# Performance work log

Measured on AMD Instinct MI355X. Metric: run time of the kernel, lower is better.

## Reference

```python
import jax, jax.numpy as jnp
import numpy as np

B = 1; T = 2048; H = 2048; NH = 16; KVH = 4; HD = 128; WIN = 512; SINK = 64
S = 64; NG = 4; MLP_I = 5504; CK = 4
INTER = NH * HD; CONV_DIM = INTER + 2 * NG * S; NPROJ = INTER + CONV_DIM + NH
EPS = 1e-6; MEPS = 1e-5


def rmsnorm(x, w, eps):
    return x * jax.lax.rsqrt(jnp.mean(x * x, -1, keepdims=True) + eps) * w


def rotate_half(x):
    h = x.shape[-1] // 2
    return jnp.concatenate([-x[..., h:], x[..., :h]], -1)


def setup_inputs():
    key = jax.random.key(0)
    ks = jax.random.split(key, 32)
    rn = lambda k, s, sc=0.02: jax.random.normal(k, s, dtype=jnp.float32) * sc
    inv = 1.0 / (10000.0 ** (np.arange(0, HD, 2, dtype=np.float64) / HD))
    fr = np.outer(np.arange(T), inv)
    emb = np.concatenate([fr, fr], -1)
    return {
        'hidden_states': jax.random.normal(ks[0], (B, T, H), dtype=jnp.float32),
        'cos': jnp.asarray(np.cos(emb), jnp.float32)[None],
        'sin': jnp.asarray(np.sin(emb), jnp.float32)[None],
        'ln1_w': jnp.ones((H,), jnp.float32),
        'q_w': rn(ks[1], (NH * HD, H)), 'q_b': rn(ks[2], (NH * HD,)),
        'k_w': rn(ks[3], (KVH * HD, H)), 'k_b': rn(ks[4], (KVH * HD,)),
        'v_w': rn(ks[5], (KVH * HD, H)), 'v_b': rn(ks[6], (KVH * HD,)),
        'o_w': rn(ks[7], (H, NH * HD)),
        'in_proj_w': rn(ks[8], (NPROJ, H)),
        'conv_w': rn(ks[9], (CONV_DIM, 1, CK), 0.1),
        'conv_b': rn(ks[10], (CONV_DIM,), 0.1),
        'dt_bias': rn(ks[11], (NH,), 0.5),
        'A_log': rn(ks[12], (NH,), 0.5),
        'D': rn(ks[13], (NH,), 0.5),
        'mnorm_w': jnp.ones((INTER,), jnp.float32),
        'out_proj_w': rn(ks[14], (H, INTER)),
        'ln2_w': jnp.ones((H,), jnp.float32),
        'gate_w': rn(ks[15], (MLP_I, H)),
        'up_w': rn(ks[16], (MLP_I, H)),
        'down_w': rn(ks[17], (H, MLP_I)),
    }


def _mamba2(ev, in_proj_w, conv_w, conv_b, dt_bias, A_log, D, mnorm_w, out_proj_w):
    # ev: [B, L, H] evicted hidden states; Mamba2 with expand=1 (intermediate=INTER)
    L = ev.shape[1]
    proj = jnp.einsum('blh,ph->blp', ev, in_proj_w)
    z = proj[..., :INTER]
    xBC = proj[..., INTER:INTER + CONV_DIM]
    dt = proj[..., INTER + CONV_DIM:]
    # depthwise causal conv1d, kernel 4
    xBC = jax.lax.conv_general_dilated(
        xBC.transpose(0, 2, 1), conv_w, (1,), [(CK - 1, 0)],
        dimension_numbers=('NCH', 'OIH', 'NCH'), feature_group_count=CONV_DIM)
    xBC = jax.nn.silu((xBC + conv_b[None, :, None]).transpose(0, 2, 1))
    x = xBC[..., :INTER].reshape(B, L, NH, HD)
    Bm = jnp.repeat(xBC[..., INTER:INTER + NG * S].reshape(B, L, NG, S), NH // NG, axis=2)
    Cm = jnp.repeat(xBC[..., INTER + NG * S:].reshape(B, L, NG, S), NH // NG, axis=2)
    dt = jax.nn.softplus(dt + dt_bias)  # [B, L, NH]
    A = -jnp.exp(A_log)  # [NH]

    def scan_one(xb, bb, cb, db):
        def step(state, inp):
            xt, bt, ct, dtt = inp  # [NH,HD],[NH,S],[NH,S],[NH]
            decay = jnp.exp(dtt * A)[:, None, None]
            state = decay * state + (dtt[:, None] * xt)[..., None] * bt[:, None, :]
            y = jnp.einsum('hds,hs->hd', state, ct) + D[:, None] * xt
            return state, y
        _, ys = jax.lax.scan(step, jnp.zeros((NH, HD, S), xb.dtype), (xb, bb, cb, db))
        return ys

    y = jax.vmap(scan_one)(x, Bm, Cm, dt).reshape(B, L, INTER)
    g = y * jax.nn.silu(z)  # gated RMSNorm
    g = g * jax.lax.rsqrt(jnp.mean(g * g, -1, keepdims=True) + MEPS) * mnorm_w
    return jnp.einsum('bli,hi->blh', g, out_proj_w)


def reference(hidden_states, cos, sin, ln1_w, q_w, q_b, k_w, k_b, v_w, v_b, o_w,
              in_proj_w, conv_w, conv_b, dt_bias, A_log, D, mnorm_w, out_proj_w,
              ln2_w, gate_w, up_w, down_w):
    pre = rmsnorm(hidden_states, ln1_w, EPS)  # input_layernorm
    evict_end = T - WIN
    mem_out = _mamba2(pre[:, SINK:evict_end, :], in_proj_w, conv_w, conv_b,
                      dt_bias, A_log, D, mnorm_w, out_proj_w)  # [B, Le, H]
    mem_act = mem_out[:, -1:, :]

    def qkv(x, w, b, nh):
        return (jnp.einsum('blh,ph->blp', x, w) + b).reshape(x.shape[0], x.shape[1], nh, HD).transpose(0, 2, 1, 3)

    q = qkv(pre, q_w, q_b, NH)
    k = qkv(pre, k_w, k_b, KVH)
    v = qkv(pre, v_w, v_b, KVH)
    c = cos[:, None]; s = sin[:, None]
    q = q * c + rotate_half(q) * s
    k = k * c + rotate_half(k) * s
    # mem token injection at position SINK (mem projections are not rotated)
    q = q.at[:, :, SINK, :].set(qkv(mem_act, q_w, q_b, NH)[:, :, 0, :])
    k = k.at[:, :, SINK, :].set(qkv(mem_act, k_w, k_b, KVH)[:, :, 0, :])
    v = v.at[:, :, SINK, :].set(qkv(mem_act, v_w, v_b, KVH)[:, :, 0, :])
    # sink + sliding-window causal mask with mem-token bias
    row = jnp.arange(T)[:, None]; col = jnp.arange(T)[None, :]
    protected = SINK + 1
    bad = (col > row) | ((col < row - WIN) & (col >= protected))
    minv = jnp.finfo(jnp.float32).min
    mask = jnp.where(bad, minv, 0.0)[None, None]
    le_fact = (T - SINK - WIN) / T
    mask = mask.at[..., SINK].add(0.5 * le_fact)
    rep = NH // KVH
    kf = jnp.repeat(k, rep, axis=1)
    vf = jnp.repeat(v, rep, axis=1)
    scores = jnp.einsum('bhqd,bhkd->bhqk', q, kf) * (HD ** -0.5) + mask
    attn = jax.nn.softmax(scores, axis=-1)
    o = jnp.einsum('bhqk,bhkd->bhqd', attn, vf).transpose(0, 2, 1, 3).reshape(B, T, NH * HD)
    # training-path merge: sinks | mem_out | window
    merged = jnp.concatenate([o[:, :SINK], mem_out, o[:, T - WIN:]], axis=1)
    attn_out = jnp.einsum('blp,hp->blh', merged, o_w)
    h = hidden_states + attn_out
    m = rmsnorm(h, ln2_w, EPS)
    mlp = jnp.einsum('bli,hi->blh',
                     jax.nn.silu(jnp.einsum('blh,ih->bli', m, gate_w)) * jnp.einsum('blh,ih->bli', m, up_w),
                     down_w)
    return h + mlp
```

## Files before the change

### kernel.cpp

```cpp
#include <hip/hip_runtime.h>
#include <hip/hip_bf16.h>

#define TSEQ   2048
#define HDIM   2048
#define NHEAD  16
#define KVHEAD 4
#define HEADD  128
#define WINSZ  512
#define SINKN  64
#define MLPI   5504
#define CONVD  2560
#define NPROJD 4624
#define LMEM   1472
#define NCHUNK 23
#define QKVD   3072

typedef unsigned short bf_t;
typedef __attribute__((ext_vector_type(8))) short short8;
typedef __attribute__((ext_vector_type(4))) short s4v;
typedef __attribute__((ext_vector_type(4))) float ffrag;

#define BOF_PRE   0ull
#define BOF_QKV   8388608ull
#define BOF_P     8388608ull
#define BOF_S     20447232ull
#define BOF_PROJ  33554432ull
#define BOF_GB    33554432ull
#define BOF_XBCC  60780544ull
#define BOF_GF    75853824ull
#define BOF_MERG  75853824ull
#define BOF_GN    87912448ull
#define BOF_H     93941760ull
#define BOF_DT    110718976ull
#define BOF_GA    110813184ull
#define BOF_FLAG  110907392ull
#define BOF_LC    110908416ull

#define BOF_CNV_A 8388608ull
#define BOF_CNV_B 60780544ull

__device__ __forceinline__ float bf2f(bf_t x) { return __uint_as_float(((unsigned)x) << 16); }
__device__ __forceinline__ bf_t f2bf(float x) {
  unsigned u = __float_as_uint(x);
  return (bf_t)((u + 0x7FFFu + ((u >> 16) & 1u)) >> 16);
}
__device__ __forceinline__ float ldin(const void* p, size_t i, int bf) {
  if (bf) return bf2f(((const bf_t*)p)[i]);
  return ((const float*)p)[i];
}
__device__ __forceinline__ float siluf(float x) { return x / (1.f + expf(-x)); }

typedef const __attribute__((address_space(1))) unsigned gl_u32;
typedef __attribute__((address_space(3))) unsigned lds_u32;
__device__ __forceinline__ void gld16(const void* g, void* l) {
  __builtin_amdgcn_global_load_lds((gl_u32*)g, (lds_u32*)l, 16, 0, 0);
}

__device__ __forceinline__ void xcd_swz(int gx, int gy, int& x, int& y) {
  int id = blockIdx.y * gx + blockIdx.x;
  int total = gx * gy;
  int xcd = id & 7, j = id >> 3;
  int q = total >> 3, r = total & 7;
  int w = (xcd < r ? xcd*(q+1) : r*(q+1) + (xcd-r)*q) + j;
  x = w / gy;
  y = w % gy;
}

__global__ void detect_k(const void* __restrict__ ln1, int* __restrict__ flag) {
  unsigned w0 = *(const unsigned*)ln1;
  *flag = (w0 == 0x3F803F80u) ? 1 : 0;
}

__global__ __launch_bounds__(256) void wconv_k(const float* __restrict__ src,
    bf_t* __restrict__ dst, int n8, const int* __restrict__ flagp) {
  if (*flagp) return;
  int idx = blockIdx.x*256 + threadIdx.x;
  if (idx >= n8) return;
  const float* s = src + (size_t)idx*8;
  float4 a = *(const float4*)s, b = *(const float4*)(s+4);
  short8 o;
  o[0]=(short)f2bf(a.x); o[1]=(short)f2bf(a.y); o[2]=(short)f2bf(a.z); o[3]=(short)f2bf(a.w);
  o[4]=(short)f2bf(b.x); o[5]=(short)f2bf(b.y); o[6]=(short)f2bf(b.z); o[7]=(short)f2bf(b.w);
  *(short8*)(dst + (size_t)idx*8) = o;
}

__global__ __launch_bounds__(256) void rms_in_k(const void* __restrict__ x,
    const void* __restrict__ w, bf_t* __restrict__ out, float eps,
    const int* __restrict__ flagp) {
  int bf = *flagp;
  int row = blockIdx.x, tid = threadIdx.x;
  float v[8];
  if (bf) {
    const bf_t* xr = (const bf_t*)x + (size_t)row*HDIM + tid*8;
#pragma unroll
    for (int j = 0; j < 8; ++j) v[j] = bf2f(xr[j]);
  } else {
    const float* xr = (const float*)x + (size_t)row*HDIM + tid*8;
    float4 a = *(const float4*)xr, b = *(const float4*)(xr+4);
    v[0]=a.x; v[1]=a.y; v[2]=a.z; v[3]=a.w; v[4]=b.x; v[5]=b.y; v[6]=b.z; v[7]=b.w;
  }
  float ss = 0.f;
#pragma unroll
  for (int j = 0; j < 8; ++j) ss += v[j]*v[j];
  __shared__ float red[256];
  red[tid] = ss; __syncthreads();
  for (int s = 128; s > 0; s >>= 1) { if (tid < s) red[tid] += red[tid+s]; __syncthreads(); }
  float scale = 1.f / sqrtf(red[0]*(1.f/HDIM) + eps);
  bf_t* o = out + (size_t)row*HDIM + tid*8;
#pragma unroll
  for (int j = 0; j < 8; ++j) o[j] = f2bf(v[j]*scale*ldin(w, tid*8+j, bf));
}

__global__ __launch_bounds__(256) void rms_f2b_k(const float* __restrict__ x,
    const void* __restrict__ w, bf_t* __restrict__ out, float eps,
    const int* __restrict__ flagp) {
  int bf = *flagp;
  int row = blockIdx.x, tid = threadIdx.x;
  const float* xr = x + (size_t)row*2048 + tid*8;
  float4 a = *(const float4*)xr, b = *(const float4*)(xr+4);
  float v[8] = {a.x,a.y,a.z,a.w,b.x,b.y,b.z,b.w};
  float ss = 0.f;
#pragma unroll
  for (int j = 0; j < 8; ++j) ss += v[j]*v[j];
  __shared__ float red[256];
  red[tid] = ss; __syncthreads();
  for (int s = 128; s > 0; s >>= 1) { if (tid < s) red[tid] += red[tid+s]; __syncthreads(); }
  float scale = 1.f / sqrtf(red[0]*(1.f/2048.f) + eps);
  bf_t* o = out + (size_t)row*2048 + tid*8;
#pragma unroll
  for (int j = 0; j < 8; ++j) o[j] = f2bf(v[j]*scale*ldin(w, tid*8+j, bf));
}

__global__ __launch_bounds__(256) void tgemm_k(
    const bf_t* __restrict__ A, int lda,
    const void* __restrict__ W0, const void* __restrict__ W1, const void* __restrict__ W2,
    const bf_t* __restrict__ C0, const bf_t* __restrict__ C1, const bf_t* __restrict__ C2,
    int ldw, int n1, int n2,
    const void* __restrict__ b0, const void* __restrict__ b1, const void* __restrict__ b2,
    const void* __restrict__ res,
    const float* __restrict__ hf,
    void* __restrict__ out,
    int ldc, int M, int N, int K, int mode, int outbf,
    const int* __restrict__ flagp) {
  int bf = *flagp;
  __shared__ short As[8192];
  __shared__ short Bs[4096];
  int tid = threadIdx.x;
  int lane = tid & 63, wv = tid >> 6;
  int sx, sy; xcd_swz(gridDim.x, gridDim.y, sx, sy);
  int bm = sy << 7, bn = sx << 6;

  int trow = tid >> 2;
  int kc = (((tid & 3) ^ ((tid >> 3) & 3)) << 3);
  int ar0 = bm + trow;        if (ar0 > M-1) ar0 = M-1;
  int ar1 = bm + 64 + trow;   if (ar1 > M-1) ar1 = M-1;
  int wr  = bn + trow;        if (wr > N-1) wr = N-1;
  const bf_t* ga0 = A + (size_t)ar0*lda + kc;
  const bf_t* ga1 = A + (size_t)ar1*lda + kc;
  const bf_t* w0 = bf ? (const bf_t*)W0 : C0;
  const bf_t* w1 = bf ? (const bf_t*)W1 : C1;
  const bf_t* w2 = bf ? (const bf_t*)W2 : C2;
  const bf_t* Wsel; int wrl;
  if (wr < n1)      { Wsel = w0; wrl = wr; }
  else if (wr < n2) { Wsel = w1; wrl = wr - n1; }
  else              { Wsel = w2; wrl = wr - n2; }
  const bf_t* gwb = Wsel + (size_t)wrl*ldw + kc;
  int sA = wv*512;

  int wm = (wv & 1) << 6, wn = (wv >> 1) << 5;
  int fr = lane & 15;
  int fq = (((lane >> 4) ^ ((fr >> 1) & 3)) << 3);

  ffrag acc[4][2];
#pragma unroll
  for (int i = 0; i < 4; ++i)
#pragma unroll
    for (int j = 0; j < 2; ++j) acc[i][j] = (ffrag){0.f,0.f,0.f,0.f};

  int nst = K >> 5;
  gld16(ga0, As + sA);
  gld16(ga1, As + 2048 + sA);
  gld16(gwb, Bs + sA);
  gld16(ga0 + 32, As + 4096 + sA);
  gld16(ga1 + 32, As + 4096 + 2048 + sA);
  gld16(gwb + 32, Bs + 2048 + sA);

  for (int t = 0; t < nst; ++t) {
    if (t + 1 < nst) { asm volatile("s_waitcnt vmcnt(3)" ::: "memory"); }
    else             { asm volatile("s_waitcnt vmcnt(0)" ::: "memory"); }
    __builtin_amdgcn_s_barrier();
    int cbA = (t & 1) << 12, cbB = (t & 1) << 11;
    short8 af[4], bfr[2];
#pragma unroll
    for (int i = 0; i < 4; ++i)
      af[i] = *(const short8*)&As[cbA + (wm + i*16 + fr)*32 + fq];
#pragma unroll
    for (int j = 0; j < 2; ++j)
      bfr[j] = *(const short8*)&Bs[cbB + (wn + j*16 + fr)*32 + fq];
    asm volatile("s_waitcnt lgkmcnt(0)" ::: "memory");
    __builtin_amdgcn_s_barrier();
    int nxt = (t + 2) << 5;
    if (nxt < K) {
      gld16(ga0 + nxt, As + cbA + sA);
      gld16(ga1 + nxt, As + cbA + 2048 + sA);
      gld16(gwb + nxt, Bs + cbB + sA);
    }
#pragma unroll
    for (int i = 0; i < 4; ++i)
#pragma unroll
      for (int j = 0; j < 2; ++j)
        acc[i][j] = __builtin_amdgcn_mfma_f32_16x16x32_bf16(af[i], bfr[j], acc[i][j], 0, 0, 0);
  }

  int rbase = (lane >> 4) << 2;
  int cbase = lane & 15;
#pragma unroll
  for (int i = 0; i < 4; ++i) {
#pragma unroll
    for (int j = 0; j < 2; ++j) {
#pragma unroll
      for (int r = 0; r < 4; ++r) {
        int m = bm + wm + i*16 + rbase + r;
        int n = bn + wn + j*16 + cbase;
        if (m >= M || n >= N) continue;
        size_t ci = (size_t)m*ldc + n;
        float v = acc[i][j][r];
        if (mode == 0) {
          if (b0) {
            if (n < n1)      v += ldin(b0, n, bf);
            else if (n < n2) v += ldin(b1, n - n1, bf);
            else             v += ldin(b2, n - n2, bf);
          }
          if (outbf) ((bf_t*)out)[ci] = f2bf(v); else ((float*)out)[ci] = v;
        } else if (mode == 1) {
          ((float*)out)[ci] = v + ldin(res, ci, bf);
        } else {
          float hv = hf[ci] + v;
          if (bf) ((bf_t*)out)[ci] = f2bf(hv); else ((float*)out)[ci] = hv;
        }
      }
    }
  }
}

__global__ __launch_bounds__(256, 2) void fgemm_k(
    const bf_t* __restrict__ A, int lda,
    const void* __restrict__ Wg, const void* __restrict__ Wu,
    const bf_t* __restrict__ Cg, const bf_t* __restrict__ Cu, int ldw,
    bf_t* __restrict__ out, int M, int N, int K,
    const int* __restrict__ flagp) {
  int bf = *flagp;
  __shared__ short As[8192];
  __shared__ short Bg[8192];
  __shared__ short Bu[8192];
  int tid = threadIdx.x;
  int lane = tid & 63, wv = tid >> 6;
  int sx, sy; xcd_swz(gridDim.x, gridDim.y, sx, sy);
  int bm = sy << 7, bn = sx << 7;

  int trow = tid >> 2;
  int kc = (((tid & 3) ^ ((tid >> 3) & 3)) << 3);
  int ar0 = bm + trow;        if (ar0 > M-1) ar0 = M-1;
  int ar1 = bm + 64 + trow;   if (ar1 > M-1) ar1 = M-1;
  const bf_t* ga0 = A + (size_t)ar0*lda + kc;
  const bf_t* ga1 = A + (size_t)ar1*lda + kc;
  const bf_t* wg = bf ? (const bf_t*)Wg : Cg;
  const bf_t* wu = bf ? (const bf_t*)Wu : Cu;
  const bf_t* gg0 = wg + (size_t)(bn + trow)*ldw + kc;
  const bf_t* gg1 = wg + (size_t)(bn + 64 + trow)*ldw + kc;
  const bf_t* gu0 = wu + (size_t)(bn + trow)*ldw + kc;
  const bf_t* gu1 = wu + (size_t)(bn + 64 + trow)*ldw + kc;
  int sA = wv*512;

  int wm = (wv & 1) << 6, wn = (wv >> 1) << 6;
  int fr = lane & 15;
  int fq = (((lane >> 4) ^ ((fr >> 1) & 3)) << 3);

  ffrag ag[4][4], au[4][4];
#pragma unroll
  for (int i = 0; i < 4; ++i)
#pragma unroll
    for (int j = 0; j < 4; ++j) { ag[i][j] = (ffrag){0.f,0.f,0.f,0.f}; au[i][j] = (ffrag){0.f,0.f,0.f,0.f}; }

  int nst = K >> 5;
  gld16(ga0, As + sA);
  gld16(ga1, As + 2048 + sA);
  gld16(gg0, Bg + sA);
  gld16(gg1, Bg + 2048 + sA);
  gld16(gu0, Bu + sA);
  gld16(gu1, Bu + 2048 + sA);
  gld16(ga0 + 32, As + 4096 + sA);
  gld16(ga1 + 32, As + 4096 + 2048 + sA);
  gld16(gg0 + 32, Bg + 4096 + sA);
  gld16(gg1 + 32, Bg + 4096 + 2048 + sA);
  gld16(gu0 + 32, Bu + 4096 + sA);
  gld16(gu1 + 32, Bu + 4096 + 2048 + sA);

  for (int t = 0; t < nst; ++t) {
    if (t + 1 < nst) { asm volatile("s_waitcnt vmcnt(6)" ::: "memory"); }
    else             { asm volatile("s_waitcnt vmcnt(0)" ::: "memory"); }
    __builtin_amdgcn_s_barrier();
    int cb = (t & 1) << 12;
    short8 af[4], bgf[4], buf2[4];
#pragma unroll
    for (int i = 0; i < 4; ++i)
      af[i] = *(const short8*)&As[cb + (wm + i*16 + fr)*32 + fq];
#pragma unroll
    for (int j = 0; j < 4; ++j) {
      bgf[j]  = *(const short8*)&Bg[cb + (wn + j*16 + fr)*32 + fq];
      buf2[j] = *(const short8*)&Bu[cb + (wn + j*16 + fr)*32 + fq];
    }
    asm volatile("s_waitcnt lgkmcnt(0)" ::: "memory");
    __builtin_amdgcn_s_barrier();
    int nxt = (t + 2) << 5;
    if (nxt < K) {
      gld16(ga0 + nxt, As + cb + sA);
      gld16(ga1 + nxt, As + cb + 2048 + sA);
      gld16(gg0 + nxt, Bg + cb + sA);
      gld16(gg1 + nxt, Bg + cb + 2048 + sA);
      gld16(gu0 + nxt, Bu + cb + sA);
      gld16(gu1 + nxt, Bu + cb + 2048 + sA);
    }
#pragma unroll
    for (int i = 0; i < 4; ++i)
#pragma unroll
      for (int j = 0; j < 4; ++j) {
        ag[i][j] = __builtin_amdgcn_mfma_f32_16x16x32_bf16(af[i], bgf[j],  ag[i][j], 0, 0, 0);
        au[i][j] = __builtin_amdgcn_mfma_f32_16x16x32_bf16(af[i], buf2[j], au[i][j], 0, 0, 0);
      }
  }

  int rbase = (lane >> 4) << 2;
  int cbase = lane & 15;
#pragma unroll
  for (int i = 0; i < 4; ++i)
#pragma unroll
    for (int j = 0; j < 4; ++j)
#pragma unroll
      for (int r = 0; r < 4; ++r) {
        int m = bm + wm + i*16 + rbase + r;
        int n = bn + wn + j*16 + cbase;
        if (m >= M || n >= N) continue;
        float g = ag[i][j][r], u = au[i][j][r];
        out[(size_t)m*N + n] = f2bf(siluf(g) * u);
      }
}

__global__ __launch_bounds__(256) void rope_k(float* __restrict__ tb, int stride,
    const void* __restrict__ cosp, const void* __restrict__ sinp,
    int nheads, const int* __restrict__ flagp) {
  int bf = *flagp;
  int idx = blockIdx.x*256 + threadIdx.x;
  int d = idx & 63;
  int rem = idx >> 6;
  int tpos = rem / nheads, hh = rem % nheads;
  float* base = tb + (size_t)tpos*stride + hh*128;
  float a = base[d], b = base[d+64];
  float c0 = ldin(cosp, (size_t)tpos*128 + d, bf),    s0 = ldin(sinp, (size_t)tpos*128 + d, bf);
  float c1 = ldin(cosp, (size_t)tpos*128 + d + 64, bf), s1 = ldin(sinp, (size_t)tpos*128 + d + 64, bf);
  base[d]    = a*c0 - b*s0;
  base[d+64] = b*c1 + a*s1;
}

__global__ __launch_bounds__(256) void conv_k(const float* __restrict__ proj,
    const void* __restrict__ convw, const void* __restrict__ convb,
    float* __restrict__ xbcc, const int* __restrict__ flagp) {
  int bf = *flagp;
  int idx = blockIdx.x*256 + threadIdx.x;
  int t = idx / CONVD, c = idx % CONVD;
  float acc = ldin(convb, c, bf);
#pragma unroll
  for (int j = 0; j < 4; ++j) {
    int tt = t - 3 + j;
    if (tt >= 0) acc += ldin(convw, (size_t)c*4 + j, bf) * proj[(size_t)tt*NPROJD + 2048 + c];
  }
  xbcc[idx] = siluf(acc);
}

__global__ __launch_bounds__(256) void dt_k(const float* __restrict__ proj,
    const void* __restrict__ dtb, const void* __restrict__ alog,
    float* __restrict__ dtv, float* __restrict__ ga, const int* __restrict__ flagp) {
  int bf = *flagp;
  int idx = blockIdx.x*256 + threadIdx.x;
  int t = idx >> 4, h = idx & 15;
  float raw = proj[(size_t)t*NPROJD + 4608 + h] + ldin(dtb, h, bf);
  float dt = (raw > 30.f) ? raw : log1pf(expf(raw));
  float A = -expf(ldin(alog, h, bf));
  dtv[idx] = dt;
  ga[idx] = dt*A;
}

__global__ __launch_bounds__(256) void cums_k(const float* __restrict__ ga,
    float* __restrict__ Lc) {
  int wid = blockIdx.x*4 + (threadIdx.x >> 6);
  int lane = threadIdx.x & 63;
  int h = wid / NCHUNK, c = wid % NCHUNK;
  int t = c*64 + lane;
  float a = ga[(size_t)t*16 + h];
#pragma unroll
  for (int off = 1; off < 64; off <<= 1) {
    float o = __shfl_up(a, off, 64);
    if (lane >= off) a += o;
  }
  Lc[(size_t)(h*NCHUNK + c)*64 + lane] = a;
}

__global__ __launch_bounds__(256) void chunkstate_k(
    const float* __restrict__ xbcc, const float* __restrict__ dtv,
    const float* __restrict__ Lc, float* __restrict__ Pbuf) {
  __shared__ short XT[128*72];
  __shared__ short BT[64*72];
  __shared__ float wj[64];
  int tid = threadIdx.x, lane = tid & 63, wv = tid >> 6;
  int b = blockIdx.x;
  int h = b & 15, c = b >> 4;
  int g64 = (h >> 2) << 6;
  size_t hc = (size_t)(h*NCHUNK + c);

  if (tid < 64) {
    float L63 = Lc[hc*64 + 63];
    float Lj  = Lc[hc*64 + tid];
    wj[tid] = dtv[(size_t)(c*64 + tid)*16 + h] * expf(L63 - Lj);
  }
  __syncthreads();
  for (int base = tid*4; base < 8192; base += 1024) {
    int j = base >> 7, d = base & 127;
    float4 xv = *(const float4*)&xbcc[(size_t)(c*64 + j)*CONVD + h*128 + d];
    XT[(d+0)*72 + j] = (short)f2bf(xv.x);
    XT[(d+1)*72 + j] = (short)f2bf(xv.y);
    XT[(d+2)*72 + j] = (short)f2bf(xv.z);
    XT[(d+3)*72 + j] = (short)f2bf(xv.w);
  }
  for (int base = tid*4; base < 4096; base += 1024) {
    int j = base >> 6, s = base & 63;
    float w = wj[j];
    float4 bv = *(const float4*)&xbcc[(size_t)(c*64 + j)*CONVD + 2048 + g64 + s];
    BT[(s+0)*72 + j] = (short)f2bf(bv.x * w);
    BT[(s+1)*72 + j] = (short)f2bf(bv.y * w);
    BT[(s+2)*72 + j] = (short)f2bf(bv.z * w);
    BT[(s+3)*72 + j] = (short)f2bf(bv.w * w);
  }
  __syncthreads();

  int fr = lane & 15, fq = (lane >> 4) << 3;
  ffrag acc[2][4];
#pragma unroll
  for (int i = 0; i < 2; ++i)
#pragma unroll
    for (int j = 0; j < 4; ++j) acc[i][j] = (ffrag){0.f,0.f,0.f,0.f};
#pragma unroll
  for (int k0 = 0; k0 < 64; k0 += 32) {
    short8 af[2], bfr[4];
#pragma unroll
    for (int i = 0; i < 2; ++i)
      af[i] = *(const short8*)&XT[(wv*32 + i*16 + fr)*72 + k0 + fq];
#pragma unroll
    for (int j = 0; j < 4; ++j)
      bfr[j] = *(const short8*)&BT[(j*16 + fr)*72 + k0 + fq];
#pragma unroll
    for (int i = 0; i < 2; ++i)
#pragma unroll
      for (int j = 0; j < 4; ++j)
        acc[i][j] = __builtin_amdgcn_mfma_f32_16x16x32_bf16(af[i], bfr[j], acc[i][j], 0, 0, 0);
  }
  int rbase = (lane >> 4) << 2, cbase = lane & 15;
#pragma unroll
  for (int i = 0; i < 2; ++i)
#pragma unroll
    for (int j = 0; j < 4; ++j)
#pragma unroll
      for (int r = 0; r < 4; ++r) {
        int d = wv*32 + i*16 + rbase + r;
        int s = j*16 + cbase;
        Pbuf[hc*8192 + d*64 + s] = acc[i][j][r];
      }
}

__global__ __launch_bounds__(256) void statepass_k(
    const float* __restrict__ Pbuf, const float* __restrict__ Lc,
    float* __restrict__ Sbuf) {
  int gid = blockIdx.x*256 + threadIdx.x;
  int h = gid >> 13, rem = gid & 8191;
  float s = 0.f;
  for (int c = 0; c < NCHUNK; ++c) {
    size_t hc = (size_t)(h*NCHUNK + c);
    Sbuf[hc*8192 + rem] = s;
    s = expf(Lc[hc*64 + 63]) * s + Pbuf[hc*8192 + rem];
  }
}

__global__ __launch_bounds__(256) void chunkout_k(
    const float* __restrict__ xbcc, const float* __restrict__ proj,
    const float* __restrict__ dtv, const float* __restrict__ Lc,
    const float* __restrict__ Sbuf, const void* __restrict__ Dp,
    float* __restrict__ g, const int* __restrict__ flagp) {
  __shared__ short Cs[64*72];
  __shared__ short BsS[64*72];
  __shared__ short XT[128*72];
  __shared__ short Sinb[128*72];
  __shared__ float Lch[64];
  __shared__ float dtch[64];
  int bf = *flagp;
  int tid = threadIdx.x, lane = tid & 63, wv = tid >> 6;
  int b = blockIdx.x;
  int h = b & 15, c = b >> 4;
  int g64 = (h >> 2) << 6;
  size_t hc = (size_t)(h*NCHUNK + c);
  float Dh = ldin(Dp, h, bf);

  if (tid < 64) {
    Lch[tid]  = Lc[hc*64 + tid];
    dtch[tid] = dtv[(size_t)(c*64 + tid)*16 + h];
  }
  for (int base = tid*4; base < 4096; base += 1024) {
    int i = base >> 6, s = base & 63;
    float4 cv = *(const float4*)&xbcc[(size_t)(c*64 + i)*CONVD + 2304 + g64 + s];
    Cs[i*72 + s+0] = (short)f2bf(cv.x); Cs[i*72 + s+1] = (short)f2bf(cv.y);
    Cs[i*72 + s+2] = (short)f2bf(cv.z); Cs[i*72 + s+3] = (short)f2bf(cv.w);
    float4 bv = *(const float4*)&xbcc[(size_t)(c*64 + i)*CONVD + 2048 + g64 + s];
    BsS[i*72 + s+0] = (short)f2bf(bv.x); BsS[i*72 + s+1] = (short)f2bf(bv.y);
    BsS[i*72 + s+2] = (short)f2bf(bv.z); BsS[i*72 + s+3] = (short)f2bf(bv.w);
  }
  for (int base = tid*4; base < 8192; base += 1024) {
    int j = base >> 7, d = base & 127;
    float4 xv = *(const float4*)&xbcc[(size_t)(c*64 + j)*CONVD + h*128 + d];
    XT[(d+0)*72 + j] = (short)f2bf(xv.x);
    XT[(d+1)*72 + j] = (short)f2bf(xv.y);
    XT[(d+2)*72 + j] = (short)f2bf(xv.z);
    XT[(d+3)*72 + j] = (short)f2bf(xv.w);
  }
  for (int base = tid*4; base < 8192; base += 1024) {
    int d = base >> 6, s = base & 63;
    float4 sv = *(const float4*)&Sbuf[hc*8192 + d*64 + s];
    Sinb[d*72 + s+0] = (short)f2bf(sv.x); Sinb[d*72 + s+1] = (short)f2bf(sv.y);
    Sinb[d*72 + s+2] = (short)f2bf(sv.z); Sinb[d*72 + s+3] = (short)f2bf(sv.w);
  }
  __syncthreads();

  int fr = lane & 15, fq = (lane >> 4) << 3;
  ffrag s0[4];
#pragma unroll
  for (int i = 0; i < 4; ++i) s0[i] = (ffrag){0.f,0.f,0.f,0.f};
#pragma unroll
  for (int k0 = 0; k0 < 64; k0 += 32) {
    short8 bfr = *(const short8*)&BsS[(wv*16 + fr)*72 + k0 + fq];
#pragma unroll
    for (int i = 0; i < 4; ++i) {
      short8 af = *(const short8*)&Cs[(i*16 + fr)*72 + k0 + fq];
      s0[i] = __builtin_amdgcn_mfma_f32_16x16x32_bf16(af, bfr, s0[i], 0, 0, 0);
    }
  }
  __syncthreads();

  {
    int rbase = (lane >> 4) << 2, cbase = lane & 15;
    int j = wv*16 + cbase;
#pragma unroll
    for (int i = 0; i < 4; ++i)
#pragma unroll
      for (int r = 0; r < 4; ++r) {
        int ii = i*16 + rbase + r;
        float v = (j <= ii) ? s0[i][r] * expf(Lch[ii] - Lch[j]) * dtch[j] : 0.f;
        BsS[ii*72 + j] = (short)f2bf(v);
      }
#pragma unroll
    for (int e = 0; e < 16; ++e) {
      int idx = tid*16 + e;
      int ii = idx >> 6, s = idx & 63;
      Cs[ii*72 + s] = (short)f2bf(bf2f((bf_t)Cs[ii*72 + s]) * expf(Lch[ii]));
    }
  }
  __syncthreads();

  ffrag acc[4][2];
#pragma unroll
  for (int i = 0; i < 4; ++i)
#pragma unroll
    for (int j = 0; j < 2; ++j) acc[i][j] = (ffrag){0.f,0.f,0.f,0.f};
#pragma unroll
  for (int k0 = 0; k0 < 64; k0 += 32) {
    short8 xb[2], af[4];
#pragma unroll
    for (int j = 0; j < 2; ++j)
      xb[j] = *(const short8*)&XT[(wv*32 + j*16 + fr)*72 + k0 + fq];
#pragma unroll
    for (int i = 0; i < 4; ++i)
      af[i] = *(const short8*)&BsS[(i*16 + fr)*72 + k0 + fq];
#pragma unroll
    for (int i = 0; i < 4; ++i)
#pragma unroll
      for (int j = 0; j < 2; ++j)
        acc[i][j] = __builtin_amdgcn_mfma_f32_16x16x32_bf16(af[i], xb[j], acc[i][j], 0, 0, 0);
  }
#pragma unroll
  for (int k0 = 0; k0 < 64; k0 += 32) {
    short8 sb[2], af[4];
#pragma unroll
    for (int j = 0; j < 2; ++j)
      sb[j] = *(const short8*)&Sinb[(wv*32 + j*16 + fr)*72 + k0 + fq];
#pragma unroll
    for (int i = 0; i < 4; ++i)
      af[i] = *(const short8*)&Cs[(i*16 + fr)*72 + k0 + fq];
#pragma unroll
    for (int i = 0; i < 4; ++i)
#pragma unroll
      for (int j = 0; j < 2; ++j)
        acc[i][j] = __builtin_amdgcn_mfma_f32_16x16x32_bf16(af[i], sb[j], acc[i][j], 0, 0, 0);
  }

  int rbase = (lane >> 4) << 2, cbase = lane & 15;
#pragma unroll
  for (int i = 0; i < 4; ++i)
#pragma unroll
    for (int j = 0; j < 2; ++j)
#pragma unroll
      for (int r = 0; r < 4; ++r) {
        int ii = i*16 + rbase + r;
        int d = wv*32 + j*16 + cbase;
        int t = c*64 + ii;
        int col = h*128 + d;
        float x = xbcc[(size_t)t*CONVD + col];
        float z = proj[(size_t)t*NPROJD + col];
        float y = acc[i][j][r] + Dh*x;
        g[(size_t)t*2048 + col] = y * siluf(z);
      }
}

__global__ __launch_bounds__(256) void memact_k(
    const bf_t* __restrict__ merged,
    const void* __restrict__ qw, const void* __restrict__ qb,
    const void* __restrict__ kw, const void* __restrict__ kb,
    const void* __restrict__ vw, const void* __restrict__ vb,
    const bf_t* __restrict__ cq, const bf_t* __restrict__ ck, const bf_t* __restrict__ cv,
    float* __restrict__ qkv, const int* __restrict__ flagp) {
  int bf = *flagp;
  int p = blockIdx.x, tid = threadIdx.x;
  const bf_t* ma = merged + (size_t)1535*2048;
  const void* b; const bf_t* wb; int off;
  if (p < 2048)      { wb = bf ? (const bf_t*)qw : cq; b = qb; off = p; }
  else if (p < 2560) { wb = bf ? (const bf_t*)kw : ck; b = kb; off = p - 2048; }
  else               { wb = bf ? (const bf_t*)vw : cv; b = vb; off = p - 2560; }
  float partial = 0.f;
  size_t wbase = (size_t)off*2048;
  for (int j = tid; j < 2048; j += 256) partial += bf2f(ma[j])*bf2f(wb[wbase + j]);
  __shared__ float red[256];
  red[tid] = partial; __syncthreads();
  for (int s = 128; s > 0; s >>= 1) { if (tid < s) red[tid] += red[tid+s]; __syncthreads(); }
  if (tid == 0) qkv[(size_t)64*QKVD + p] = red[0] + ldin(b, off, bf);
}

__global__ __launch_bounds__(256) void attn3_k(
    const float* __restrict__ qkv, bf_t* __restrict__ merged) {
  __shared__ short Qs[64*136];
  __shared__ short Ks[64*136];
  __shared__ short Vt[128*72];
  __shared__ short Pb[64*72];

  int bid = blockIdx.x;
  int g = bid & 3, hg = (bid >> 2) & 3, qt = bid >> 4;
  int r0 = (qt == 0) ? 0 : (1536 + 64*(qt-1));
  int tid = threadIdx.x, lane = tid & 63, wv = tid >> 6;

  int qcol = g*512 + hg*128;
  int kcol = 2048 + g*128;
  int vcol = 2560 + g*128;

  int fr = lane & 15, fq = (lane >> 4) << 3;
  int rloc = (lane >> 4) << 2;
  int cb = lane & 15;

  {
    int row = tid >> 2, c4 = tid & 3;
    const float* qp = qkv + (size_t)(r0 + row)*QKVD + qcol;
#pragma unroll
    for (int rep = 0; rep < 8; ++rep) {
      int d = (c4 + rep*4)*4;
      float4 v = *(const float4*)(qp + d);
      s4v o;
      o[0] = (short)f2bf(v.x); o[1] = (short)f2bf(v.y);
      o[2] = (short)f2bf(v.z); o[3] = (short)f2bf(v.w);
      *(s4v*)&Qs[row*136 + d] = o;
    }
  }
  __syncthreads();

  float m4[4] = {-3.0e38f, -3.0e38f, -3.0e38f, -3.0e38f};
  float l4[4] = {0.f, 0.f, 0.f, 0.f};
  ffrag o8[8];
#pragma unroll
  for (int n = 0; n < 8; ++n) o8[n] = (ffrag){0.f,0.f,0.f,0.f};

  int ntiles = (qt == 0) ? 1 : 11;
  for (int t = 0; t < ntiles; ++t) {
    int kb = (t == 0) ? 0 : ((t == 1) ? 64 : (r0 - 512 + 64*(t-2)));

    {
      int row = tid >> 2, c4 = tid & 3;
      const float* kp = qkv + (size_t)(kb + row)*QKVD + kcol;
#pragma unroll
      for (int rep = 0; rep < 8; ++rep) {
        int d = (c4 + rep*4)*4;
        float4 v = *(const float4*)(kp + d);
        s4v o;
        o[0] = (short)f2bf(v.x); o[1] = (short)f2bf(v.y);
        o[2] = (short)f2bf(v.z); o[3] = (short)f2bf(v.w);
        *(s4v*)&Ks[row*136 + d] = o;
      }
    }
#pragma unroll
    for (int it = 0; it < 8; ++it) {
      int task = tid + it*256;
      int d = task & 127, jg = task >> 7;
      const float* vp = qkv + (size_t)(kb + jg*4)*QKVD + vcol + d;
      s4v o;
      o[0] = (short)f2bf(vp[0]);
      o[1] = (short)f2bf(vp[QKVD]);
      o[2] = (short)f2bf(vp[2*QKVD]);
      o[3] = (short)f2bf(vp[3*QKVD]);
      *(s4v*)&Vt[d*72 + jg*4] = o;
    }
    __syncthreads();

    ffrag s[4];
#pragma unroll
    for (int n = 0; n < 4; ++n) s[n] = (ffrag){0.f,0.f,0.f,0.f};
#pragma unroll
    for (int k0 = 0; k0 < 128; k0 += 32) {
      short8 aq = *(const short8*)&Qs[(wv*16 + fr)*136 + k0 + fq];
#pragma unroll
      for (int n = 0; n < 4; ++n) {
        short8 bk = *(const short8*)&Ks[(n*16 + fr)*136 + k0 + fq];
        s[n] = __builtin_amdgcn_mfma_f32_16x16x32_bf16(aq, bk, s[n], 0, 0, 0);
      }
    }

    float tmax[4] = {-INFINITY, -INFINITY, -INFINITY, -INFINITY};
#pragma unroll
    for (int n = 0; n < 4; ++n) {
      int kk = kb + n*16 + cb;
      float bias = (kk == 64) ? 0.359375f : 0.f;
#pragma unroll
      for (int rg = 0; rg < 4; ++rg) {
        int rr = r0 + wv*16 + rloc + rg;
        bool ok = (kk <= rr) && ((kk >= rr - 512) || (kk < 65));
        float sv = ok ? (s[n][rg]*0.08838834764831845f + bias) : -INFINITY;
        s[n][rg] = sv;
        tmax[rg] = fmaxf(tmax[rg], sv);
      }
    }
    float sc4[4];
#pragma unroll
    for (int rg = 0; rg < 4; ++rg) {
#pragma unroll
      for (int off = 1; off < 16; off <<= 1)
        tmax[rg] = fmaxf(tmax[rg], __shfl_xor(tmax[rg], off, 64));
      float mnew = fmaxf(m4[rg], tmax[rg]);
      sc4[rg] = expf(m4[rg] - mnew);
      m4[rg] = mnew;
      l4[rg] *= sc4[rg];
    }
#pragma unroll
    for (int n = 0; n < 8; ++n)
#pragma unroll
      for (int rg = 0; rg < 4; ++rg) o8[n][rg] *= sc4[rg];

    float ts[4] = {0.f, 0.f, 0.f, 0.f};
#pragma unroll
    for (int n = 0; n < 4; ++n)
#pragma unroll
      for (int rg = 0; rg < 4; ++rg) {
        float p = expf(s[n][rg] - m4[rg]);
        ts[rg] += p;
        Pb[(wv*16 + rloc + rg)*72 + n*16 + cb] = (short)f2bf(p);
      }
#pragma unroll
    for (int rg = 0; rg < 4; ++rg) {
#pragma unroll
      for (int off = 1; off < 16; off <<= 1) ts[rg] += __shfl_xor(ts[rg], off, 64);
      l4[rg] += ts[rg];
    }

#pragma unroll
    for (int k0 = 0; k0 < 64; k0 += 32) {
      short8 ap = *(const short8*)&Pb[(wv*16 + fr)*72 + k0 + fq];
#pragma unroll
      for (int n = 0; n < 8; ++n) {
        short8 bv = *(const short8*)&Vt[(n*16 + fr)*72 + k0 + fq];
        o8[n] = __builtin_amdgcn_mfma_f32_16x16x32_bf16(ap, bv, o8[n], 0, 0, 0);
      }
    }
    __syncthreads();
  }

  float inv[4];
#pragma unroll
  for (int rg = 0; rg < 4; ++rg) inv[rg] = 1.f / l4[rg];
#pragma unroll
  for (int n = 0; n < 8; ++n)
#pragma unroll
    for (int rg = 0; rg < 4; ++rg) {
      int i = wv*16 + rloc + rg;
      int d = n*16 + cb;
      merged[(size_t)(r0 + i)*2048 + (g*4 + hg)*128 + d] = f2bf(o8[n][rg]*inv[rg]);
    }
}

extern "C" void kernel_launch(void* const* d_in, const int* in_sizes, int n_in,
                              void* d_out, int out_size, void* d_ws, size_t ws_size,
                              hipStream_t stream) {
  const void* hidden = d_in[0];
  const void* cosp   = d_in[1];
  const void* sinp   = d_in[2];
  const void* ln1w   = d_in[3];
  const void* qw = d_in[4];  const void* qb = d_in[5];
  const void* kw = d_in[6];  const void* kb = d_in[7];
  const void* vw = d_in[8];  const void* vb = d_in[9];
  const void* ow = d_in[10];
  const void* inpw = d_in[11];
  const void* convw = d_in[12]; const void* convb = d_in[13];
  const void* dtb = d_in[14]; const void* alog = d_in[15]; const void* dd = d_in[16];
  const void* mnw = d_in[17]; const void* outpw = d_in[18];
  const void* ln2w = d_in[19];
  const void* gatew = d_in[20]; const void* upw = d_in[21]; const void* downw = d_in[22];

  char* wsb = (char*)d_ws;
  bf_t*  pre    = (bf_t*)(wsb + BOF_PRE);
  bf_t*  mbuf   = (bf_t*)(wsb + BOF_PRE);
  float* qkv    = (float*)(wsb + BOF_QKV);
  float* Pbuf   = (float*)(wsb + BOF_P);
  float* Sbuf   = (float*)(wsb + BOF_S);
  float* proj   = (float*)(wsb + BOF_PROJ);
  bf_t*  Gbuf   = (bf_t*)(wsb + BOF_GB);
  float* xbcc   = (float*)(wsb + BOF_XBCC);
  float* gbuf   = (float*)(wsb + BOF_GF);
  bf_t*  merged = (bf_t*)(wsb + BOF_MERG);
  bf_t*  gn     = (bf_t*)(wsb + BOF_GN);
  float* hbuf   = (float*)(wsb + BOF_H);
  float* dtv    = (float*)(wsb + BOF_DT);
  float* ga     = (float*)(wsb + BOF_GA);
  int*   flag   = (int*)(wsb + BOF_FLAG);
  float* Lc     = (float*)(wsb + BOF_LC);
  bf_t*  cvA    = (bf_t*)(wsb + BOF_CNV_A);
  bf_t*  cvB    = (bf_t*)(wsb + BOF_CNV_B);
  bf_t*  cvq    = cvB;
  bf_t*  cvk    = cvB + 4194304;
  bf_t*  cvv    = cvB + 5242880;

  detect_k<<<dim3(1), dim3(1), 0, stream>>>(ln1w, flag);
  rms_in_k<<<dim3(TSEQ), dim3(256), 0, stream>>>(hidden, ln1w, pre, 1e-6f, flag);

  wconv_k<<<dim3(4624), dim3(256), 0, stream>>>((const float*)inpw, cvA, 1183744, flag);
  tgemm_k<<<dim3(73,12), dim3(256), 0, stream>>>(pre + (size_t)64*2048, 2048,
      inpw, nullptr, nullptr, cvA, nullptr, nullptr, 2048, NPROJD, NPROJD,
      nullptr, nullptr, nullptr,
      nullptr, nullptr, proj, NPROJD, LMEM, NPROJD, 2048, 0, 0, flag);
  conv_k<<<dim3((LMEM*CONVD)/256), dim3(256), 0, stream>>>(proj, convw, convb, xbcc, flag);
  dt_k<<<dim3((LMEM*16)/256), dim3(256), 0, stream>>>(proj, dtb, alog, dtv, ga, flag);
  cums_k<<<dim3(92), dim3(256), 0, stream>>>(ga, Lc);
  chunkstate_k<<<dim3(368), dim3(256), 0, stream>>>(xbcc, dtv, Lc, Pbuf);
  statepass_k<<<dim3(512), dim3(256), 0, stream>>>(Pbuf, Lc, Sbuf);
  wconv_k<<<dim3(2048), dim3(256), 0, stream>>>((const float*)outpw, cvA, 524288, flag);
  chunkout_k<<<dim3(368), dim3(256), 0, stream>>>(xbcc, proj, dtv, Lc, Sbuf, dd, gbuf, flag);
  rms_f2b_k<<<dim3(LMEM), dim3(256), 0, stream>>>(gbuf, mnw, gn, 1e-5f, flag);
  tgemm_k<<<dim3(32,12), dim3(256), 0, stream>>>(gn, 2048,
      outpw, nullptr, nullptr, cvA, nullptr, nullptr, 2048, 2048, 2048,
      nullptr, nullptr, nullptr,
      nullptr, nullptr, merged + (size_t)64*2048, 2048, LMEM, 2048, 2048, 0, 1, flag);

  wconv_k<<<dim3(2048), dim3(256), 0, stream>>>((const float*)qw, cvq, 524288, flag);
  wconv_k<<<dim3(512),  dim3(256), 0, stream>>>((const float*)kw, cvk, 131072, flag);
  wconv_k<<<dim3(512),  dim3(256), 0, stream>>>((const float*)vw, cvv, 131072, flag);
  tgemm_k<<<dim3(48,16), dim3(256), 0, stream>>>(pre, 2048,
      qw, kw, vw, cvq, cvk, cvv, 2048, 2048, 2560, qb, kb, vb,
      nullptr, nullptr, qkv, QKVD, 2048, QKVD, 2048, 0, 0, flag);
  rope_k<<<dim3(8192), dim3(256), 0, stream>>>(qkv, QKVD, cosp, sinp, 16, flag);
  rope_k<<<dim3(2048), dim3(256), 0, stream>>>(qkv + 2048, QKVD, cosp, sinp, 4, flag);

  memact_k<<<dim3(3072), dim3(256), 0, stream>>>(merged, qw, qb, kw, kb, vw, vb,
      cvq, cvk, cvv, qkv, flag);
  attn3_k<<<dim3(144), dim3(256), 0, stream>>>(qkv, merged);

  wconv_k<<<dim3(2048), dim3(256), 0, stream>>>((const float*)ow, cvB, 524288, flag);
  tgemm_k<<<dim3(32,16), dim3(256), 0, stream>>>(merged, 2048,
      ow, nullptr, nullptr, cvB, nullptr, nullptr, 2048, 2048, 2048,
      nullptr, nullptr, nullptr,
      hidden, nullptr, hbuf, 2048, 2048, 2048, 2048, 1, 0, flag);
  rms_f2b_k<<<dim3(TSEQ), dim3(256), 0, stream>>>(hbuf, ln2w, mbuf, 1e-6f, flag);

  wconv_k<<<dim3(5504), dim3(256), 0, stream>>>((const float*)gatew, cvA, 1409024, flag);
  wconv_k<<<dim3(5504), dim3(256), 0, stream>>>((const float*)upw,   cvB, 1409024, flag);
  fgemm_k<<<dim3(43,16), dim3(256), 0, stream>>>(mbuf, 2048, gatew, upw, cvA, cvB, 2048,
      Gbuf, 2048, MLPI, 2048, flag);
  wconv_k<<<dim3(5504), dim3(256), 0, stream>>>((const float*)downw, cvA, 1409024, flag);
  tgemm_k<<<dim3(32,16), dim3(256), 0, stream>>>(Gbuf, MLPI,
      downw, nullptr, nullptr, cvA, nullptr, nullptr, MLPI, 2048, 2048,
      nullptr, nullptr, nullptr,
      nullptr, hbuf, d_out, 2048, 2048, 2048, MLPI, 3, 0, flag);
}
```

Baseline: 628.4 us.

## Triple-buffer shared memory tiles in GEMM kernels to issue loads earlier

Switches the tgemm and fgemm main loops from double to triple-buffered LDS staging. The load for tile t+2 is now issued at the top of each iteration, before waiting for tile t, and the vmcnt thresholds are relaxed so more global loads stay in flight. This aims to hide global memory latency behind MFMA work. It raises LDS usage per block, which may reduce the number of resident blocks per CU.

After: 660.3 us. 1.05x slower.

```diff
diff --git a/kernel.cpp b/kernel.cpp
--- a/kernel.cpp
+++ b/kernel.cpp
@@ -143,8 +143,8 @@
     int ldc, int M, int N, int K, int mode, int outbf,
     const int* __restrict__ flagp) {
   int bf = *flagp;
-  __shared__ short As[8192];
-  __shared__ short Bs[4096];
+  __shared__ short As[12288];
+  __shared__ short Bs[6144];
   int tid = threadIdx.x;
   int lane = tid & 63, wv = tid >> 6;
   int sx, sy; xcd_swz(gridDim.x, gridDim.y, sx, sy);
@@ -185,11 +185,21 @@
   gld16(ga1 + 32, As + 4096 + 2048 + sA);
   gld16(gwb + 32, Bs + 2048 + sA);
 
+  int s0 = 0;
   for (int t = 0; t < nst; ++t) {
-    if (t + 1 < nst) { asm volatile("s_waitcnt vmcnt(3)" ::: "memory"); }
-    else             { asm volatile("s_waitcnt vmcnt(0)" ::: "memory"); }
+    int s2 = s0 + 2; if (s2 >= 3) s2 -= 3;
+    int nxt = (t + 2) << 5;
+    if (nxt < K) {
+      int a2 = s2 << 12, b2o = s2 << 11;
+      gld16(ga0 + nxt, As + a2 + sA);
+      gld16(ga1 + nxt, As + a2 + 2048 + sA);
+      gld16(gwb + nxt, Bs + b2o + sA);
+    }
+    if (t + 2 < nst)      { asm volatile("s_waitcnt vmcnt(6)" ::: "memory"); }
+    else if (t + 1 < nst) { asm volatile("s_waitcnt vmcnt(3)" ::: "memory"); }
+    else                  { asm volatile("s_waitcnt vmcnt(0)" ::: "memory"); }
     __builtin_amdgcn_s_barrier();
-    int cbA = (t & 1) << 12, cbB = (t & 1) << 11;
+    int cbA = s0 << 12, cbB = s0 << 11;
     short8 af[4], bfr[2];
 #pragma unroll
     for (int i = 0; i < 4; ++i)
@@ -199,17 +209,12 @@
       bfr[j] = *(const short8*)&Bs[cbB + (wn + j*16 + fr)*32 + fq];
     asm volatile("s_waitcnt lgkmcnt(0)" ::: "memory");
     __builtin_amdgcn_s_barrier();
-    int nxt = (t + 2) << 5;
-    if (nxt < K) {
-      gld16(ga0 + nxt, As + cbA + sA);
-      gld16(ga1 + nxt, As + cbA + 2048 + sA);
-      gld16(gwb + nxt, Bs + cbB + sA);
-    }
 #pragma unroll
     for (int i = 0; i < 4; ++i)
 #pragma unroll
       for (int j = 0; j < 2; ++j)
         acc[i][j] = __builtin_amdgcn_mfma_f32_16x16x32_bf16(af[i], bfr[j], acc[i][j], 0, 0, 0);
+    s0 = s0 + 1; if (s0 >= 3) s0 = 0;
   }
 
   int rbase = (lane >> 4) << 2;
@@ -250,9 +255,9 @@
     bf_t* __restrict__ out, int M, int N, int K,
     const int* __restrict__ flagp) {
   int bf = *flagp;
-  __shared__ short As[8192];
-  __shared__ short Bg[8192];
-  __shared__ short Bu[8192];
+  __shared__ short As[12288];
+  __shared__ short Bg[12288];
+  __shared__ short Bu[12288];
   int tid = threadIdx.x;
   int lane = tid & 63, wv = tid >> 6;
   int sx, sy; xcd_swz(gridDim.x, gridDim.y, sx, sy);
@@ -296,11 +301,24 @@
   gld16(gu0 + 32, Bu + 4096 + sA);
   gld16(gu1 + 32, Bu + 4096 + 2048 + sA);
 
+  int s0 = 0;
   for (int t = 0; t < nst; ++t) {
-    if (t + 1 < nst) { asm volatile("s_waitcnt vmcnt(6)" ::: "memory"); }
-    else             { asm volatile("s_waitcnt vmcnt(0)" ::: "memory"); }
+    int s2 = s0 + 2; if (s2 >= 3) s2 -= 3;
+    int nxt = (t + 2) << 5;
+    if (nxt < K) {
+      int c2 = s2 << 12;
+      gld16(ga0 + nxt, As + c2 + sA);
+      gld16(ga1 + nxt, As + c2 + 2048 + sA);
+      gld16(gg0 + nxt, Bg + c2 + sA);
+      gld16(gg1 + nxt, Bg + c2 + 2048 + sA);
+      gld16(gu0 + nxt, Bu + c2 + sA);
+      gld16(gu1 + nxt, Bu + c2 + 2048 + sA);
+    }
+    if (t + 2 < nst)      { asm volatile("s_waitcnt vmcnt(12)" ::: "memory"); }
+    else if (t + 1 < nst) { asm volatile("s_waitcnt vmcnt(6)" ::: "memory"); }
+    else                  { asm volatile("s_waitcnt vmcnt(0)" ::: "memory"); }
     __builtin_amdgcn_s_barrier();
-    int cb = (t & 1) << 12;
+    int cb = s0 << 12;
     short8 af[4], bgf[4], buf2[4];
 #pragma unroll
     for (int i = 0; i < 4; ++i)
@@ -312,15 +330,6 @@
     }
     asm volatile("s_waitcnt lgkmcnt(0)" ::: "memory");
     __builtin_amdgcn_s_barrier();
-    int nxt = (t + 2) << 5;
-    if (nxt < K) {
-      gld16(ga0 + nxt, As + cb + sA);
-      gld16(ga1 + nxt, As + cb + 2048 + sA);
-      gld16(gg0 + nxt, Bg + cb + sA);
-      gld16(gg1 + nxt, Bg + cb + 2048 + sA);
-      gld16(gu0 + nxt, Bu + cb + sA);
-      gld16(gu1 + nxt, Bu + cb + 2048 + sA);
-    }
 #pragma unroll
     for (int i = 0; i < 4; ++i)
 #pragma unroll
@@ -328,6 +337,7 @@
         ag[i][j] = __builtin_amdgcn_mfma_f32_16x16x32_bf16(af[i], bgf[j],  ag[i][j], 0, 0, 0);
         au[i][j] = __builtin_amdgcn_mfma_f32_16x16x32_bf16(af[i], buf2[j], au[i][j], 0, 0, 0);
       }
+    s0 = s0 + 1; if (s0 >= 3) s0 = 0;
   }
 
   int rbase = (lane >> 4) << 2;
```
